# Kernel optimization log

Hardware: AMD Instinct MI355X
Metric: run time of the kernel (lower is better)

## Reference

```python
import jax, jax.numpy as jnp
import numpy as np

B, S, D, H = 2, 2048, 1024, 16
DK = D // H  # 64

def setup_inputs() -> dict:
    key = jax.random.key(0)
    ks = jax.random.split(key, 12)
    scale = 1.0 / np.sqrt(D)
    return {
        "q": jax.random.normal(ks[0], (B, S, D), jnp.float32),
        "k": jax.random.normal(ks[1], (B, S, D), jnp.float32),
        "v": jax.random.normal(ks[2], (B, S, D), jnp.float32),
        "Wq": jax.random.normal(ks[3], (D, D), jnp.float32) * scale,
        "bq": jnp.zeros((D,), jnp.float32),
        "Wk": jax.random.normal(ks[4], (D, D), jnp.float32) * scale,
        "bk": jnp.zeros((D,), jnp.float32),
        "Wv": jax.random.normal(ks[5], (D, D), jnp.float32) * scale,
        "bv": jnp.zeros((D,), jnp.float32),
        "Wo": jax.random.normal(ks[6], (D, D), jnp.float32) * scale,
        "bo": jnp.zeros((D,), jnp.float32),
        "mask": jnp.ones((B, 1, S, S), jnp.bool_),
    }

def reference(q, k, v, Wq, bq, Wk, bk, Wv, bv, Wo, bo, mask):
    # Linear projections: y = x @ W^T + b (torch nn.Linear convention)
    def proj(x, W, b):
        return x @ W.T + b
    # [B,S,D] -> [B,H,S,DK]
    def split_heads(x):
        return x.reshape(B, S, H, DK).transpose(0, 2, 1, 3)

    query = split_heads(proj(q, Wq, bq))
    key_ = split_heads(proj(k, Wk, bk))
    value = split_heads(proj(v, Wv, bv))

    # NOTE: original uses out-of-place masked_fill whose result is discarded,
    # so mask has no effect on the computation (reproduced faithfully here).
    scores = jnp.einsum('bhqd,bhkd->bhqk', query, key_) / jnp.sqrt(
        jnp.asarray(DK, query.dtype))
    attn = jax.nn.softmax(scores, axis=-1)  # dropout p=0.0: identity
    x = jnp.einsum('bhqk,bhkd->bhqd', attn, value)
    x = x.transpose(0, 2, 1, 3).reshape(B, S, D)
    return proj(x, Wo, bo)
```

## Files before the change

kernel.cpp:

```cpp
#include <hip/hip_runtime.h>
#include <hip/hip_bf16.h>


typedef __attribute__((ext_vector_type(8))) short bf16x8;
typedef __attribute__((ext_vector_type(4))) float f32x4;
typedef unsigned short u16;
typedef unsigned int u32;

#define MFMA16(a, b, c) __builtin_amdgcn_mfma_f32_16x16x32_bf16(a, b, c, 0, 0, 0)
#define EXP2(x) __builtin_amdgcn_exp2f(x)

static __device__ __forceinline__ u16 f2bf(float f) {
    union { __hip_bfloat16 h; u16 u; } v;
    v.h = __float2bfloat16(f);
    return v.u;
}

static __device__ __forceinline__ u16 f2bf_fast(float f) {
    return (u16)((__float_as_uint(f) + 0x8000u) >> 16);
}

static __device__ __forceinline__ void gload16(const u16* g, u16* l) {
    __builtin_amdgcn_global_load_lds(
        (const __attribute__((address_space(1))) void*)g,
        (__attribute__((address_space(3))) void*)l, 16, 0, 0);
}

struct CvtArgs16 { const float* in[16]; u16* out[16]; };

__global__ __launch_bounds__(256)
void cvt_multi(CvtArgs16 a)
{
    const int tsel = blockIdx.x >> 9;
    const int i = (((blockIdx.x & 511) * 256) + threadIdx.x) * 8;
    const float* in = a.in[tsel];
    u16* out = a.out[tsel];
    float4 x = *(const float4*)(in + i);
    float4 y = *(const float4*)(in + i + 4);
    u16 o[8];
    o[0]=f2bf(x.x); o[1]=f2bf(x.y); o[2]=f2bf(x.z); o[3]=f2bf(x.w);
    o[4]=f2bf(y.x); o[5]=f2bf(y.y); o[6]=f2bf(y.z); o[7]=f2bf(y.w);
    *(uint4*)(out + i) = *(uint4*)o;
}

struct GemmArgs {
    const u16* A[3]; const u16* W[3]; const float* bias[3];
    u16* C[3]; float osc[3]; int epi[3];
};

__global__ __launch_bounds__(256)
void gemm_qkv(GemmArgs g)
{
    __shared__ u16 lds_a[2][128 * 32];
    __shared__ u16 lds_b[2][128 * 32];

    const int z = blockIdx.y;
    const u16* Ap = g.A[z];
    const u16* Wp = g.W[z];
    const int epi = g.epi[z];

    const int t    = threadIdx.x;
    const int lane = t & 63;
    const int w    = t >> 6;
    const int wm   = w >> 1, wn = w & 1;
    const int ll   = lane & 15;
    const int lg   = lane >> 4;

    const int bx  = blockIdx.x;
    const int swz = (bx & 7) * 32 + (bx >> 3);
    const int tile_m = (epi == 1 ? (swz & 7) : (swz >> 3)) * 128;
    const int tile_n = (epi == 1 ? (swz >> 3) : (swz & 7)) * 128;

    const int c0   = w * 2;
    const int lrow = lane >> 2;
    const int lcol = (lane & 3) * 8;

    f32x4 acc[4][4] = {};

    #define STAGE(buf, kt)                                                     \
    {                                                                          \
        _Pragma("unroll")                                                      \
        for (int j = 0; j < 2; j++) {                                          \
            const int c = c0 + j;                                              \
            gload16(Ap + (size_t)(tile_m + c * 16 + lrow) * 1024 + (kt) + lcol,\
                    &lds_a[buf][c * 512]);                                     \
            gload16(Wp + (size_t)(tile_n + c * 16 + lrow) * 1024 + (kt) + lcol,\
                    &lds_b[buf][c * 512]);                                     \
        }                                                                      \
    }

    STAGE(0, 0);
    __syncthreads();

    int cur = 0;
    for (int kt = 0; kt < 1024; kt += 32) {
        if (kt + 32 < 1024) STAGE(cur ^ 1, kt + 32);

        bf16x8 af[4], bfr[4];
        #pragma unroll
        for (int i = 0; i < 4; i++)
            af[i] = *(bf16x8*)&lds_a[cur][(wm * 64 + i * 16 + ll) * 32 + lg * 8];
        #pragma unroll
        for (int j = 0; j < 4; j++)
            bfr[j] = *(bf16x8*)&lds_b[cur][(wn * 64 + j * 16 + ll) * 32 + lg * 8];
        #pragma unroll
        for (int i = 0; i < 4; i++)
            #pragma unroll
            for (int j = 0; j < 4; j++)
                acc[i][j] = MFMA16(af[i], bfr[j], acc[i][j]);

        __syncthreads();
        cur ^= 1;
    }
    #undef STAGE

    const float osc = g.osc[z];
    const float* bias = g.bias[z];
    u16* Cp = g.C[z];

    #pragma unroll
    for (int i = 0; i < 4; i++) {
        const int row0 = tile_m + wm * 64 + i * 16 + lg * 4;
        #pragma unroll
        for (int j = 0; j < 4; j++) {
            const int col = tile_n + wn * 64 + j * 16 + ll;
            if (epi == 1) {
                const int b = col >> 11, s = col & 2047;
                #pragma unroll
                for (int r = 0; r < 4; r++)
                    Cp[(size_t)(b * 1024 + row0 + r) * 2048 + s] =
                        f2bf(acc[i][j][r] + bias[row0 + r]);
            } else {
                const float bias_v = bias[col];
                const int h = col >> 6, dk = col & 63;
                const int b = row0 >> 11;
                #pragma unroll
                for (int r = 0; r < 4; r++) {
                    const int s = (row0 + r) & 2047;
                    Cp[((size_t)(b * 16 + h) * 2048 + s) * 64 + dk] =
                        f2bf((acc[i][j][r] + bias_v) * osc);
                }
            }
        }
    }
}

__global__ __launch_bounds__(256)
void gemm_out(const u16* __restrict__ Ap, const u16* __restrict__ Wp,
              const float* __restrict__ bias, float* __restrict__ Cp)
{
    __shared__ u16 lds_a[2][128 * 32];
    __shared__ u16 lds_b[2][64 * 32];

    const int t    = threadIdx.x;
    const int lane = t & 63;
    const int w    = t >> 6;
    const int wm   = w >> 1, wn = w & 1;
    const int ll   = lane & 15;
    const int lg   = lane >> 4;

    const int bx  = blockIdx.x;
    const int swz = (bx & 7) * 64 + (bx >> 3);
    const int tile_m = (swz >> 4) * 128;
    const int tile_n = (swz & 15) * 64;

    const int lrow = lane >> 2;
    const int lcol = (lane & 3) * 8;

    f32x4 acc[4][2] = {};

    #define OSTAGE(buf, kt)                                                    \
    {                                                                          \
        _Pragma("unroll")                                                      \
        for (int j = 0; j < 3; j++) {                                          \
            const int c = w * 3 + j;                                           \
            if (c < 8) {                                                       \
                const int row = tile_m + c * 16 + lrow;                        \
                const int col = (kt) + lcol;                                   \
                const u16* ga = Ap + ((size_t)((row >> 11) * 16 + (col >> 6))  \
                                      * 2048 + (row & 2047)) * 64 + (col & 63);\
                gload16(ga, &lds_a[buf][c * 512]);                             \
            } else {                                                           \
                const int cc = c - 8;                                          \
                gload16(Wp + (size_t)(tile_n + cc * 16 + lrow) * 1024          \
                        + (kt) + lcol, &lds_b[buf][cc * 512]);                 \
            }                                                                  \
        }                                                                      \
    }

    OSTAGE(0, 0);
    __syncthreads();

    int cur = 0;
    for (int kt = 0; kt < 1024; kt += 32) {
        if (kt + 32 < 1024) OSTAGE(cur ^ 1, kt + 32);

        bf16x8 af[4], bfr[2];
        #pragma unroll
        for (int i = 0; i < 4; i++)
            af[i] = *(bf16x8*)&lds_a[cur][(wm * 64 + i * 16 + ll) * 32 + lg * 8];
        #pragma unroll
        for (int j = 0; j < 2; j++)
            bfr[j] = *(bf16x8*)&lds_b[cur][(wn * 32 + j * 16 + ll) * 32 + lg * 8];
        #pragma unroll
        for (int i = 0; i < 4; i++)
            #pragma unroll
            for (int j = 0; j < 2; j++)
                acc[i][j] = MFMA16(af[i], bfr[j], acc[i][j]);

        __syncthreads();
        cur ^= 1;
    }
    #undef OSTAGE

    #pragma unroll
    for (int i = 0; i < 4; i++) {
        const int row0 = tile_m + wm * 64 + i * 16 + lg * 4;
        #pragma unroll
        for (int j = 0; j < 2; j++) {
            const int col = tile_n + wn * 32 + j * 16 + ll;
            const float bias_v = bias[col];
            #pragma unroll
            for (int r = 0; r < 4; r++)
                Cp[(size_t)(row0 + r) * 1024 + col] = acc[i][j][r] + bias_v;
        }
    }
}

__global__ __launch_bounds__(512)
void attn_kernel(const u16* __restrict__ Qh, const u16* __restrict__ Kh,
                 const u16* __restrict__ Vt, u16* __restrict__ Oh)
{
    __shared__ u16 lds_k[2][64 * 64];
    __shared__ u16 lds_v[2][64 * 64];
    __shared__ u16 lds_p[8][16 * 64];

    const int t    = threadIdx.x;
    const int lane = t & 63;
    const int w    = t >> 6;
    const int ll   = lane & 15;
    const int lg   = lane >> 4;
    const int r7   = ll & 7;

    const int bx  = blockIdx.x;
    const int swz = (bx & 7) * 64 + (bx >> 3);
    const int qt = swz & 15;
    const int bh = swz >> 4;
    const int q0 = qt * 128 + w * 16;

    const u16* Qbase = Qh + ((size_t)bh * 2048 + q0 + ll) * 64 + lg * 8;
    const bf16x8 bq0 = *(const bf16x8*)(Qbase);
    const bf16x8 bq1 = *(const bf16x8*)(Qbase + 32);

    bf16x8 bones;
    #pragma unroll
    for (int i = 0; i < 8; i++) bones[i] = (short)0x3F80;

    f32x4 acc[4] = {};
    f32x4 acc_l = {};

    const int srow = lane >> 3;
    const int scol = 8 * ((lane & 7) ^ srow);
    const u16* Kg = Kh + (size_t)bh * 2048 * 64;
    const u16* Vg = Vt + (size_t)bh * 64 * 2048;

    #define ASTAGE(buf, kt)                                                    \
    {                                                                          \
        const int rr = w * 8 + srow;                                           \
        gload16(Kg + (size_t)((kt) + rr) * 64 + scol, &lds_k[buf][w * 512]);   \
        gload16(Vg + (size_t)rr * 2048 + (kt) + scol, &lds_v[buf][w * 512]);   \
    }

    ASTAGE(0, 0);
    __syncthreads();

    u16* lp = lds_p[w];
    int cur = 0;

    for (int kt = 0; kt < 2048; kt += 64) {
        if (kt + 64 < 2048) ASTAGE(cur ^ 1, kt + 64);

        f32x4 s[4];
        __builtin_amdgcn_s_setprio(1);
        #pragma unroll
        for (int ks = 0; ks < 4; ks++) {
            const u16* kp = &lds_k[cur][(ks * 16 + ll) * 64];
            const bf16x8 ak0 = *(const bf16x8*)(kp + ((lg * 8)      ^ (r7 * 8)));
            const bf16x8 ak1 = *(const bf16x8*)(kp + ((lg * 8 + 32) ^ (r7 * 8)));
            f32x4 z = {0.f, 0.f, 0.f, 0.f};
            z = MFMA16(ak0, bq0, z);
            z = MFMA16(ak1, bq1, z);
            s[ks] = z;
        }
        __builtin_amdgcn_s_setprio(0);

        #pragma unroll
        for (int ks = 0; ks < 4; ks++) {
            u16 pk[4];
            #pragma unroll
            for (int r = 0; r < 4; r++) pk[r] = f2bf_fast(EXP2(s[ks][r]));
            *(uint2*)&lp[ll * 64 + ((ks * 16 + lg * 4) ^ (r7 * 8))] = *(uint2*)pk;
        }

        __builtin_amdgcn_s_setprio(1);
        #pragma unroll
        for (int ks2 = 0; ks2 < 2; ks2++) {
            const int so = (ks2 * 32 + lg * 8) ^ (r7 * 8);
            const bf16x8 pa = *(const bf16x8*)&lp[ll * 64 + so];
            #pragma unroll
            for (int dt = 0; dt < 4; dt++) {
                const bf16x8 bv = *(const bf16x8*)&lds_v[cur][(dt * 16 + ll) * 64 + so];
                acc[dt] = MFMA16(pa, bv, acc[dt]);
            }
            acc_l = MFMA16(pa, bones, acc_l);
        }
        __builtin_amdgcn_s_setprio(0);

        __syncthreads();
        cur ^= 1;
    }
    #undef ASTAGE

    #pragma unroll
    for (int r = 0; r < 4; r++) {
        const float lq = 1.f / acc_l[r];
        const int qg = q0 + lg * 4 + r;
        u16* Op = Oh + ((size_t)bh * 2048 + qg) * 64 + ll;
        #pragma unroll
        for (int dt = 0; dt < 4; dt++)
            Op[dt * 16] = f2bf(acc[dt][r] * lq);
    }
}

extern "C" void kernel_launch(void* const* d_in, const int* in_sizes, int n_in,
                              void* d_out, int out_size, void* d_ws, size_t ws_size,
                              hipStream_t stream) {
    const float* q  = (const float*)d_in[0];
    const float* k  = (const float*)d_in[1];
    const float* v  = (const float*)d_in[2];
    const float* Wq = (const float*)d_in[3];
    const float* bq = (const float*)d_in[4];
    const float* Wk = (const float*)d_in[5];
    const float* bk = (const float*)d_in[6];
    const float* Wv = (const float*)d_in[7];
    const float* bv = (const float*)d_in[8];
    const float* Wo = (const float*)d_in[9];
    const float* bo = (const float*)d_in[10];
    float* out = (float*)d_out;

    const size_t M4 = (size_t)4 * 1024 * 1024;
    const size_t M1 = (size_t)1024 * 1024;
    const float qscale = 0.18033688011112042f;
    const dim3 blk(256);

    if (ws_size >= (size_t)56 * 1024 * 1024) {
        u16* Xq  = (u16*)d_ws;
        u16* Xk  = Xq + M4;
        u16* Xv  = Xk + M4;
        u16* Qh  = Xv + M4;
        u16* Kh  = Qh + M4;
        u16* Vtb = Kh + M4;
        u16* Wqb = Vtb + M4;
        u16* Wkb = Wqb + M1;
        u16* Wvb = Wkb + M1;
        u16* Wob = Wvb + M1;
        u16* Oh  = Xq;

        CvtArgs16 cv;
        cv.in[0]=Wq; cv.out[0]=Wqb;
        cv.in[1]=Wk; cv.out[1]=Wkb;
        cv.in[2]=Wv; cv.out[2]=Wvb;
        cv.in[3]=Wo; cv.out[3]=Wob;
        for (int j = 0; j < 4; j++) {
            cv.in[4 + j]  = q + (size_t)j * M1;  cv.out[4 + j]  = Xq + (size_t)j * M1;
            cv.in[8 + j]  = k + (size_t)j * M1;  cv.out[8 + j]  = Xk + (size_t)j * M1;
            cv.in[12 + j] = v + (size_t)j * M1;  cv.out[12 + j] = Xv + (size_t)j * M1;
        }
        cvt_multi<<<16 * 512, blk, 0, stream>>>(cv);

        GemmArgs ga;
        ga.A[0]=Xq;  ga.A[1]=Xk;  ga.A[2]=Wvb;
        ga.W[0]=Wqb; ga.W[1]=Wkb; ga.W[2]=Xv;
        ga.bias[0]=bq; ga.bias[1]=bk; ga.bias[2]=bv;
        ga.C[0]=Qh; ga.C[1]=Kh; ga.C[2]=Vtb;
        ga.osc[0]=qscale; ga.osc[1]=1.0f; ga.osc[2]=1.0f;
        ga.epi[0]=3; ga.epi[1]=3; ga.epi[2]=1;
        gemm_qkv<<<dim3(256, 3), blk, 0, stream>>>(ga);

        attn_kernel<<<512, dim3(512), 0, stream>>>(Qh, Kh, Vtb, Oh);

        gemm_out<<<512, blk, 0, stream>>>(Oh, Wob, bo, out);
    } else {
        u16* X   = (u16*)d_ws;
        u16* Qh  = X + M4;
        u16* Kh  = Qh + M4;
        u16* Vtb = Kh + M4;
        u16* Wqb = Vtb + M4;
        u16* Wkb = Wqb + M1;
        u16* Wvb = Wkb + M1;
        u16* Wob = Wvb + M1;

        CvtArgs16 cw;
        for (int j = 0; j < 16; j++) { cw.in[j] = Wq; cw.out[j] = Wqb; }
        cw.in[0]=Wq; cw.out[0]=Wqb; cw.in[1]=Wk; cw.out[1]=Wkb;
        cw.in[2]=Wv; cw.out[2]=Wvb; cw.in[3]=Wo; cw.out[3]=Wob;
        cvt_multi<<<4 * 512, blk, 0, stream>>>(cw);

        const float* srcs[3] = {q, k, v};
        for (int i = 0; i < 3; i++) {
            CvtArgs16 cx;
            for (int j = 0; j < 16; j++) { cx.in[j] = srcs[i]; cx.out[j] = X; }
            for (int j = 0; j < 4; j++) {
                cx.in[j]  = srcs[i] + (size_t)j * M1;
                cx.out[j] = X + (size_t)j * M1;
            }
            cvt_multi<<<4 * 512, blk, 0, stream>>>(cx);
            GemmArgs ga;
            for (int z = 0; z < 3; z++) {
                if (i == 2) { ga.A[z]=Wvb; ga.W[z]=X;  ga.C[z]=Vtb; ga.bias[z]=bv; ga.osc[z]=1.0f; ga.epi[z]=1; }
                else if (i == 0) { ga.A[z]=X; ga.W[z]=Wqb; ga.C[z]=Qh; ga.bias[z]=bq; ga.osc[z]=qscale; ga.epi[z]=3; }
                else { ga.A[z]=X; ga.W[z]=Wkb; ga.C[z]=Kh; ga.bias[z]=bk; ga.osc[z]=1.0f; ga.epi[z]=3; }
            }
            gemm_qkv<<<dim3(256, 1), blk, 0, stream>>>(ga);
        }

        attn_kernel<<<512, dim3(512), 0, stream>>>(Qh, Kh, Vtb, X);

        gemm_out<<<512, blk, 0, stream>>>(X, Wob, bo, out);
    }
}
```

Baseline: 125.1 us.

## Fuse fp32-to-bf16 activation conversion into QKV GEMM tile loads

The QKV GEMM now reads the fp32 q/k/v activations directly, converts them to bf16 in registers, and writes them into LDS, while the bf16 weights still use async global-to-LDS loads. This removes the separate conversion pass over the three activation tensors and its bf16 staging buffers, saving a full write and re-read of about 24 MB. In exchange each GEMM tile reads fp32 activations (twice the bytes, repeated across 8 column tiles) through registers with synchronous stores to LDS, which adds register pressure and may leave fewer loads in flight than the direct-to-LDS path. The host code also drops the small-workspace fallback path.

```diff
diff --git a/kernel.cpp b/kernel.cpp
--- a/kernel.cpp
+++ b/kernel.cpp
@@ -24,6 +24,14 @@
     __builtin_amdgcn_global_load_lds(
         (const __attribute__((address_space(1))) void*)g,
         (__attribute__((address_space(3))) void*)l, 16, 0, 0);
+}
+
+static __device__ __forceinline__ void cvt16(float4 f0, float4 f1,
+                                             float4 f2, float4 f3, u16* o) {
+    o[0]=f2bf(f0.x);  o[1]=f2bf(f0.y);  o[2]=f2bf(f0.z);  o[3]=f2bf(f0.w);
+    o[4]=f2bf(f1.x);  o[5]=f2bf(f1.y);  o[6]=f2bf(f1.z);  o[7]=f2bf(f1.w);
+    o[8]=f2bf(f2.x);  o[9]=f2bf(f2.y);  o[10]=f2bf(f2.z); o[11]=f2bf(f2.w);
+    o[12]=f2bf(f3.x); o[13]=f2bf(f3.y); o[14]=f2bf(f3.z); o[15]=f2bf(f3.w);
 }
 
 struct CvtArgs16 { const float* in[16]; u16* out[16]; };
@@ -44,7 +52,7 @@
 }
 
 struct GemmArgs {
-    const u16* A[3]; const u16* W[3]; const float* bias[3];
+    const float* F[3]; const u16* Wb[3]; const float* bias[3];
     u16* C[3]; float osc[3]; int epi[3];
 };
 
@@ -55,8 +63,8 @@
     __shared__ u16 lds_b[2][128 * 32];
 
     const int z = blockIdx.y;
-    const u16* Ap = g.A[z];
-    const u16* Wp = g.W[z];
+    const float* Fp = g.F[z];
+    const u16*  Gp = g.Wb[z];
     const int epi = g.epi[z];
 
     const int t    = threadIdx.x;
@@ -71,30 +79,56 @@
     const int tile_m = (epi == 1 ? (swz & 7) : (swz >> 3)) * 128;
     const int tile_n = (epi == 1 ? (swz >> 3) : (swz & 7)) * 128;
 
+    const int rowF = (epi == 1) ? tile_n : tile_m;
+    const int rowG = (epi == 1) ? tile_m : tile_n;
+
     const int c0   = w * 2;
     const int lrow = lane >> 2;
     const int lcol = (lane & 3) * 8;
 
+    const int srow = t >> 1;
+    const int scol = (t & 1) * 16;
+    const float* Fbase = Fp + (size_t)(rowF + srow) * 1024 + scol;
+    const u16*   Gb0   = Gp + (size_t)(rowG + c0 * 16 + lrow) * 1024 + lcol;
+
     f32x4 acc[4][4] = {};
 
-    #define STAGE(buf, kt)                                                     \
-    {                                                                          \
-        _Pragma("unroll")                                                      \
-        for (int j = 0; j < 2; j++) {                                          \
-            const int c = c0 + j;                                              \
-            gload16(Ap + (size_t)(tile_m + c * 16 + lrow) * 1024 + (kt) + lcol,\
-                    &lds_a[buf][c * 512]);                                     \
-            gload16(Wp + (size_t)(tile_n + c * 16 + lrow) * 1024 + (kt) + lcol,\
-                    &lds_b[buf][c * 512]);                                     \
-        }                                                                      \
-    }
-
-    STAGE(0, 0);
+    {
+        u16* ldsG = (epi == 1) ? lds_a[0] : lds_b[0];
+        #pragma unroll
+        for (int j = 0; j < 2; j++)
+            gload16(Gb0 + (size_t)j * 16 * 1024, &ldsG[(c0 + j) * 512]);
+
+        float4 f0 = *(const float4*)(Fbase);
+        float4 f1 = *(const float4*)(Fbase + 4);
+        float4 f2 = *(const float4*)(Fbase + 8);
+        float4 f3 = *(const float4*)(Fbase + 12);
+        u16 tmp[16];
+        cvt16(f0, f1, f2, f3, tmp);
+        u16* ldsF = (epi == 1) ? lds_b[0] : lds_a[0];
+        *(uint4*)&ldsF[srow * 32 + scol]     = *(uint4*)tmp;
+        *(uint4*)&ldsF[srow * 32 + scol + 8] = *(uint4*)(tmp + 8);
+    }
     __syncthreads();
 
     int cur = 0;
     for (int kt = 0; kt < 1024; kt += 32) {
-        if (kt + 32 < 1024) STAGE(cur ^ 1, kt + 32);
+        const int nxt = cur ^ 1;
+        const bool more = (kt + 32 < 1024);
+
+        float4 f0, f1, f2, f3;
+        if (more) {
+            const float* Fs = Fbase + kt + 32;
+            f0 = *(const float4*)(Fs);
+            f1 = *(const float4*)(Fs + 4);
+            f2 = *(const float4*)(Fs + 8);
+            f3 = *(const float4*)(Fs + 12);
+            u16* ldsG = (epi == 1) ? lds_a[nxt] : lds_b[nxt];
+            #pragma unroll
+            for (int j = 0; j < 2; j++)
+                gload16(Gb0 + (size_t)j * 16 * 1024 + kt + 32,
+                        &ldsG[(c0 + j) * 512]);
+        }
 
         bf16x8 af[4], bfr[4];
         #pragma unroll
@@ -109,10 +143,17 @@
             for (int j = 0; j < 4; j++)
                 acc[i][j] = MFMA16(af[i], bfr[j], acc[i][j]);
 
+        if (more) {
+            u16 tmp[16];
+            cvt16(f0, f1, f2, f3, tmp);
+            u16* ldsF = (epi == 1) ? lds_b[nxt] : lds_a[nxt];
+            *(uint4*)&ldsF[srow * 32 + scol]     = *(uint4*)tmp;
+            *(uint4*)&ldsF[srow * 32 + scol + 8] = *(uint4*)(tmp + 8);
+        }
+
         __syncthreads();
-        cur ^= 1;
-    }
-    #undef STAGE
+        cur = nxt;
+    }
 
     const float osc = g.osc[z];
     const float* bias = g.bias[z];
@@ -353,79 +394,33 @@
     const float qscale = 0.18033688011112042f;
     const dim3 blk(256);
 
-    if (ws_size >= (size_t)56 * 1024 * 1024) {
-        u16* Xq  = (u16*)d_ws;
-        u16* Xk  = Xq + M4;
-        u16* Xv  = Xk + M4;
-        u16* Qh  = Xv + M4;
-        u16* Kh  = Qh + M4;
-        u16* Vtb = Kh + M4;
-        u16* Wqb = Vtb + M4;
-        u16* Wkb = Wqb + M1;
-        u16* Wvb = Wkb + M1;
-        u16* Wob = Wvb + M1;
-        u16* Oh  = Xq;
-
-        CvtArgs16 cv;
-        cv.in[0]=Wq; cv.out[0]=Wqb;
-        cv.in[1]=Wk; cv.out[1]=Wkb;
-        cv.in[2]=Wv; cv.out[2]=Wvb;
-        cv.in[3]=Wo; cv.out[3]=Wob;
-        for (int j = 0; j < 4; j++) {
-            cv.in[4 + j]  = q + (size_t)j * M1;  cv.out[4 + j]  = Xq + (size_t)j * M1;
-            cv.in[8 + j]  = k + (size_t)j * M1;  cv.out[8 + j]  = Xk + (size_t)j * M1;
-            cv.in[12 + j] = v + (size_t)j * M1;  cv.out[12 + j] = Xv + (size_t)j * M1;
-        }
-        cvt_multi<<<16 * 512, blk, 0, stream>>>(cv);
-
-        GemmArgs ga;
-        ga.A[0]=Xq;  ga.A[1]=Xk;  ga.A[2]=Wvb;
-        ga.W[0]=Wqb; ga.W[1]=Wkb; ga.W[2]=Xv;
-        ga.bias[0]=bq; ga.bias[1]=bk; ga.bias[2]=bv;
-        ga.C[0]=Qh; ga.C[1]=Kh; ga.C[2]=Vtb;
-        ga.osc[0]=qscale; ga.osc[1]=1.0f; ga.osc[2]=1.0f;
-        ga.epi[0]=3; ga.epi[1]=3; ga.epi[2]=1;
-        gemm_qkv<<<dim3(256, 3), blk, 0, stream>>>(ga);
-
-        attn_kernel<<<512, dim3(512), 0, stream>>>(Qh, Kh, Vtb, Oh);
-
-        gemm_out<<<512, blk, 0, stream>>>(Oh, Wob, bo, out);
-    } else {
-        u16* X   = (u16*)d_ws;
-        u16* Qh  = X + M4;
-        u16* Kh  = Qh + M4;
-        u16* Vtb = Kh + M4;
-        u16* Wqb = Vtb + M4;
-        u16* Wkb = Wqb + M1;
-        u16* Wvb = Wkb + M1;
-        u16* Wob = Wvb + M1;
-
-        CvtArgs16 cw;
-        for (int j = 0; j < 16; j++) { cw.in[j] = Wq; cw.out[j] = Wqb; }
-        cw.in[0]=Wq; cw.out[0]=Wqb; cw.in[1]=Wk; cw.out[1]=Wkb;
-        cw.in[2]=Wv; cw.out[2]=Wvb; cw.in[3]=Wo; cw.out[3]=Wob;
-        cvt_multi<<<4 * 512, blk, 0, stream>>>(cw);
-
-        const float* srcs[3] = {q, k, v};
-        for (int i = 0; i < 3; i++) {
-            CvtArgs16 cx;
-            for (int j = 0; j < 16; j++) { cx.in[j] = srcs[i]; cx.out[j] = X; }
-            for (int j = 0; j < 4; j++) {
-                cx.in[j]  = srcs[i] + (size_t)j * M1;
-                cx.out[j] = X + (size_t)j * M1;
-            }
-            cvt_multi<<<4 * 512, blk, 0, stream>>>(cx);
-            GemmArgs ga;
-            for (int z = 0; z < 3; z++) {
-                if (i == 2) { ga.A[z]=Wvb; ga.W[z]=X;  ga.C[z]=Vtb; ga.bias[z]=bv; ga.osc[z]=1.0f; ga.epi[z]=1; }
-                else if (i == 0) { ga.A[z]=X; ga.W[z]=Wqb; ga.C[z]=Qh; ga.bias[z]=bq; ga.osc[z]=qscale; ga.epi[z]=3; }
-                else { ga.A[z]=X; ga.W[z]=Wkb; ga.C[z]=Kh; ga.bias[z]=bk; ga.osc[z]=1.0f; ga.epi[z]=3; }
-            }
-            gemm_qkv<<<dim3(256, 1), blk, 0, stream>>>(ga);
-        }
-
-        attn_kernel<<<512, dim3(512), 0, stream>>>(Qh, Kh, Vtb, X);
-
-        gemm_out<<<512, blk, 0, stream>>>(X, Wob, bo, out);
-    }
-}
+    u16* Qh  = (u16*)d_ws;
+    u16* Kh  = Qh + M4;
+    u16* Vtb = Kh + M4;
+    u16* Oh  = Vtb + M4;
+    u16* Wqb = Oh + M4;
+    u16* Wkb = Wqb + M1;
+    u16* Wvb = Wkb + M1;
+    u16* Wob = Wvb + M1;
+
+    CvtArgs16 cv;
+    for (int j = 0; j < 16; j++) { cv.in[j] = Wq; cv.out[j] = Wqb; }
+    cv.in[0]=Wq; cv.out[0]=Wqb;
+    cv.in[1]=Wk; cv.out[1]=Wkb;
+    cv.in[2]=Wv; cv.out[2]=Wvb;
+    cv.in[3]=Wo; cv.out[3]=Wob;
+    cvt_multi<<<4 * 512, blk, 0, stream>>>(cv);
+
+    GemmArgs ga;
+    ga.F[0]=q;   ga.F[1]=k;   ga.F[2]=v;
+    ga.Wb[0]=Wqb; ga.Wb[1]=Wkb; ga.Wb[2]=Wvb;
+    ga.bias[0]=bq; ga.bias[1]=bk; ga.bias[2]=bv;
+    ga.C[0]=Qh; ga.C[1]=Kh; ga.C[2]=Vtb;
+    ga.osc[0]=qscale; ga.osc[1]=1.0f; ga.osc[2]=1.0f;
+    ga.epi[0]=3; ga.epi[1]=3; ga.epi[2]=1;
+    gemm_qkv<<<dim3(256, 3), blk, 0, stream>>>(ga);
+
+    attn_kernel<<<512, dim3(512), 0, stream>>>(Qh, Kh, Vtb, Oh);
+
+    gemm_out<<<512, blk, 0, stream>>>(Oh, Wob, bo, out);
+}
```

New measurement: 122.2 us (median of 2 runs). -2.3%, faster.
